# Kernel tuning notes

Measured on AMD Instinct MI355X. Metric: run time of the kernel, lower is better.

The kernel has to match this reference:

```python
import jax, jax.numpy as jnp
import numpy as np

N_HEAD = 16
N_QUERY_GROUPS = 4
HEAD_SIZE = 128
ROPE_N_ELEM = 32
N_EMBD = 2048
LN_EPS = 1e-5


def _layernorm(x, w, b):
    mu = jnp.mean(x, axis=-1, keepdims=True)
    var = jnp.var(x, axis=-1, keepdims=True)
    return (x - mu) * jax.lax.rsqrt(var + LN_EPS) * w + b


def _apply_rope(x, cos, sin):
    # x: (B, H, T, ROPE_N_ELEM); cos/sin: (T, ROPE_N_ELEM) broadcast over B,H
    half = x.shape[-1] // 2
    x1, x2 = x[..., :half], x[..., half:]
    rotated = jnp.concatenate((-x2, x1), axis=-1)
    return x * cos + rotated * sin


def setup_inputs() -> dict:
    key = jax.random.key(0)
    ks = jax.random.split(key, 12)
    B, T, C = 2, 2048, N_EMBD
    qkv_out = (N_HEAD + 2 * N_QUERY_GROUPS) * HEAD_SIZE
    ffn = 4 * C
    s = lambda fan_in: 1.0 / np.sqrt(fan_in)
    # rope cache (lit-gpt build_rope_cache, base 10000)
    theta = 1.0 / (10000.0 ** (jnp.arange(0, ROPE_N_ELEM, 2, dtype=jnp.float32) / ROPE_N_ELEM))
    idx_theta = jnp.outer(jnp.arange(T, dtype=jnp.float32), theta)  # (T, ROPE/2)
    idx_theta = jnp.concatenate((idx_theta, idx_theta), axis=-1)    # (T, ROPE)
    return {
        'x': jax.random.normal(ks[0], (B, T, C), dtype=jnp.float32),
        'cos': jnp.cos(idx_theta),
        'sin': jnp.sin(idx_theta),
        'ln1_w': jnp.ones((C,), jnp.float32),
        'ln1_b': jnp.zeros((C,), jnp.float32),
        'w_qkv': jax.random.normal(ks[1], (C, qkv_out), jnp.float32) * s(C),
        'b_qkv': jnp.zeros((qkv_out,), jnp.float32),
        'w_proj': jax.random.normal(ks[2], (C, C), jnp.float32) * s(C),
        'b_proj': jnp.zeros((C,), jnp.float32),
        'ln2_w': jnp.ones((C,), jnp.float32),
        'ln2_b': jnp.zeros((C,), jnp.float32),
        'w_fc1': jax.random.normal(ks[3], (C, ffn), jnp.float32) * s(C),
        'b_fc1': jnp.zeros((ffn,), jnp.float32),
        'w_fc2': jax.random.normal(ks[4], (ffn, C), jnp.float32) * s(ffn),
        'b_fc2': jnp.zeros((C,), jnp.float32),
    }


def reference(x, cos, sin, ln1_w, ln1_b, w_qkv, b_qkv, w_proj, b_proj,
              ln2_w, ln2_b, w_fc1, b_fc1, w_fc2, b_fc2):
    B, T, C = x.shape
    q_per_kv = N_HEAD // N_QUERY_GROUPS
    D = HEAD_SIZE

    # LayerNormLinear: fused LN + QKV projection
    qkv = _layernorm(x, ln1_w, ln1_b) @ w_qkv + b_qkv           # (B,T,(H+2G)*D)
    qkv = qkv.reshape(B, T, N_QUERY_GROUPS, q_per_kv + 2, D)
    qkv = jnp.transpose(qkv, (0, 2, 3, 1, 4))                    # (B,G,q_per_kv+2,T,D)
    q = qkv[:, :, :q_per_kv]                                     # (B,G,q_per_kv,T,D)
    k = qkv[:, :, q_per_kv:q_per_kv + 1]                         # (B,G,1,T,D)
    v = qkv[:, :, q_per_kv + 1:]
    k = jnp.broadcast_to(k, (B, N_QUERY_GROUPS, q_per_kv, T, D))
    v = jnp.broadcast_to(v, (B, N_QUERY_GROUPS, q_per_kv, T, D))
    q = q.reshape(B, N_HEAD, T, D)
    k = k.reshape(B, N_HEAD, T, D)
    v = v.reshape(B, N_HEAD, T, D)

    # inline RoPE on first ROPE_N_ELEM channels
    q = jnp.concatenate((_apply_rope(q[..., :ROPE_N_ELEM], cos, sin), q[..., ROPE_N_ELEM:]), axis=-1)
    k = jnp.concatenate((_apply_rope(k[..., :ROPE_N_ELEM], cos, sin), k[..., ROPE_N_ELEM:]), axis=-1)

    # causal scaled dot-product attention
    scale = 1.0 / jnp.sqrt(jnp.asarray(D, q.dtype))
    scores = jnp.einsum('bhtd,bhsd->bhts', q, k) * scale          # (B,H,T,T)
    causal = jnp.tril(jnp.ones((T, T), dtype=bool))
    scores = jnp.where(causal, scores, jnp.finfo(scores.dtype).min)
    probs = jax.nn.softmax(scores, axis=-1)
    y = jnp.einsum('bhts,bhsd->bhtd', probs, v)                   # (B,H,T,D)
    y = jnp.transpose(y, (0, 2, 1, 3)).reshape(B, T, C)

    h = y @ w_proj + b_proj

    # parallel residual: x + attn + LayerNormMLP(x)
    mlp_in = _layernorm(x, ln2_w, ln2_b)
    mlp = jax.nn.gelu(mlp_in @ w_fc1 + b_fc1, approximate=False) @ w_fc2 + b_fc2
    return mlp + h + x
```

## Files before the change

### kernel.cpp

```cpp
#include <hip/hip_runtime.h>
#include <cstdint>
#include <cstddef>


typedef unsigned short u16;
typedef __bf16 bf16x8 __attribute__((ext_vector_type(8)));
typedef float  f32x4  __attribute__((ext_vector_type(4)));

#define B_      2
#define T_      2048
#define C_      2048
#define NH_     16
#define NG_     4
#define HD_     128
#define QKVO_   3072
#define FFN_    8192
#define ROWS_   4096

__device__ __forceinline__ u16 f2b(float f) {
  union { float f; uint32_t u; } c; c.f = f;
  uint32_t u = c.u;
  return (u16)((u + 0x7fffu + ((u >> 16) & 1u)) >> 16);
}
__device__ __forceinline__ float b2f(u16 h) {
  union { uint32_t u; float f; } c; c.u = ((uint32_t)h) << 16;
  return c.f;
}
__device__ __forceinline__ void load_lds16(const void* g, void* l) {
  __builtin_amdgcn_global_load_lds(
      (const __attribute__((address_space(1))) uint32_t*)g,
      (__attribute__((address_space(3))) uint32_t*)l, 16, 0, 0);
}

__global__ __launch_bounds__(256) void ln2x_kernel(
    const float* __restrict__ x,
    const float* __restrict__ w1, const float* __restrict__ b1,
    const float* __restrict__ w2, const float* __restrict__ b2,
    u16* __restrict__ o1, u16* __restrict__ o2)
{
  const int row = blockIdx.x;
  const float4* xr = (const float4*)(x + (size_t)row * C_);
  const int t = threadIdx.x;
  float4 v0 = xr[t];
  float4 v1 = xr[t + 256];
  float s  = v0.x + v0.y + v0.z + v0.w + v1.x + v1.y + v1.z + v1.w;
  float ss = v0.x*v0.x + v0.y*v0.y + v0.z*v0.z + v0.w*v0.w
           + v1.x*v1.x + v1.y*v1.y + v1.z*v1.z + v1.w*v1.w;
#pragma unroll
  for (int o = 32; o; o >>= 1) { s += __shfl_down(s, o); ss += __shfl_down(ss, o); }
  __shared__ float red[8];
  const int w = t >> 6;
  if ((t & 63) == 0) { red[w] = s; red[4 + w] = ss; }
  __syncthreads();
  s  = red[0] + red[1] + red[2] + red[3];
  ss = red[4] + red[5] + red[6] + red[7];
  const float mu   = s * (1.0f / C_);
  const float rstd = rsqrtf(ss * (1.0f / C_) - mu * mu + 1e-5f);

  const float4* W1 = (const float4*)w1; const float4* B1 = (const float4*)b1;
  const float4* W2 = (const float4*)w2; const float4* B2 = (const float4*)b2;
#pragma unroll
  for (int c = 0; c < 2; ++c) {
    const int idx = t + c * 256;
    float4 v = (c == 0) ? v0 : v1;
    float n0 = (v.x - mu) * rstd, n1 = (v.y - mu) * rstd;
    float n2 = (v.z - mu) * rstd, n3 = (v.w - mu) * rstd;
    float4 a1 = W1[idx], c1 = B1[idx], a2 = W2[idx], c2 = B2[idx];
    uint64_t p1 = (uint64_t)f2b(n0*a1.x + c1.x)
                | ((uint64_t)f2b(n1*a1.y + c1.y) << 16)
                | ((uint64_t)f2b(n2*a1.z + c1.z) << 32)
                | ((uint64_t)f2b(n3*a1.w + c1.w) << 48);
    uint64_t p2 = (uint64_t)f2b(n0*a2.x + c2.x)
                | ((uint64_t)f2b(n1*a2.y + c2.y) << 16)
                | ((uint64_t)f2b(n2*a2.z + c2.z) << 32)
                | ((uint64_t)f2b(n3*a2.w + c2.w) << 48);
    ((uint64_t*)o1)[(size_t)row * (C_/4) + idx] = p1;
    ((uint64_t*)o2)[(size_t)row * (C_/4) + idx] = p2;
  }
}

__global__ void tcast_kernel(const float* __restrict__ in, u16* __restrict__ out,
                             int R, int Ccols)
{
  __shared__ float tile[32][33];
  const int c0 = blockIdx.x * 32, r0 = blockIdx.y * 32;
  const int tx = threadIdx.x, ty = threadIdx.y;
#pragma unroll
  for (int i = 0; i < 4; ++i)
    tile[ty + i*8][tx] = in[(size_t)(r0 + ty + i*8) * Ccols + c0 + tx];
  __syncthreads();
#pragma unroll
  for (int i = 0; i < 4; ++i)
    out[(size_t)(c0 + ty + i*8) * R + r0 + tx] = f2b(tile[tx][ty + i*8]);
}

template <int EPI>
__global__ __launch_bounds__(256, 2) void gemm_bt(
    const u16* __restrict__ A, const u16* __restrict__ Bt,
    const float* __restrict__ bias, const float* __restrict__ resid,
    u16* __restrict__ outB, float* __restrict__ outF,
    int M, int N, int K)
{
  __shared__ u16 As[128 * 32];
  __shared__ u16 Bs[128 * 32];
  const int tid = threadIdx.x;
  const int w = tid >> 6, lane = tid & 63, quad = lane >> 4, l16 = lane & 15;
  const int wm = w >> 1, wn = w & 1;
  const int m0 = blockIdx.y * 128, n0 = blockIdx.x * 128;

  const f32x4 vzero = {0.f, 0.f, 0.f, 0.f};
  f32x4 acc[4][4];
#pragma unroll
  for (int i = 0; i < 4; ++i)
#pragma unroll
    for (int j = 0; j < 4; ++j) acc[i][j] = vzero;

  const u16* Ap = A  + (size_t)m0 * K;
  const u16* Bp = Bt + (size_t)n0 * K;
  const int rowS = tid >> 2;
  const int slotS = tid & 3;

  for (int k0 = 0; k0 < K; k0 += 32) {
    __syncthreads();
#pragma unroll
    for (int i = 0; i < 2; ++i) {
      int row = rowS + i * 64;
      int chunk = slotS ^ ((row >> 1) & 3);
      load_lds16(Ap + (size_t)row * K + k0 + chunk * 8, (char*)As + i * 4096 + w * 1024);
      load_lds16(Bp + (size_t)row * K + k0 + chunk * 8, (char*)Bs + i * 4096 + w * 1024);
    }
    __syncthreads();

    bf16x8 af[4], bf[4];
#pragma unroll
    for (int mt = 0; mt < 4; ++mt) {
      int row = wm * 64 + mt * 16 + l16;
      int slot = quad ^ ((row >> 1) & 3);
      af[mt] = *(const bf16x8*)(As + row * 32 + slot * 8);
    }
#pragma unroll
    for (int nt = 0; nt < 4; ++nt) {
      int row = wn * 64 + nt * 16 + l16;
      int slot = quad ^ ((row >> 1) & 3);
      bf[nt] = *(const bf16x8*)(Bs + row * 32 + slot * 8);
    }
#pragma unroll
    for (int mt = 0; mt < 4; ++mt)
#pragma unroll
      for (int nt = 0; nt < 4; ++nt)
        acc[mt][nt] = __builtin_amdgcn_mfma_f32_16x16x32_bf16(af[mt], bf[nt], acc[mt][nt], 0, 0, 0);
  }

#pragma unroll
  for (int mt = 0; mt < 4; ++mt)
#pragma unroll
    for (int nt = 0; nt < 4; ++nt)
#pragma unroll
      for (int r = 0; r < 4; ++r) {
        int row = m0 + wm * 64 + mt * 16 + quad * 4 + r;
        int col = n0 + wn * 64 + nt * 16 + l16;
        float v = acc[mt][nt][r] + bias[col];
        if constexpr (EPI == 1)
          v = 0.5f * v * (1.0f + erff(v * 0.70710678118654752f));
        if constexpr (EPI == 2) {
          v += resid[(size_t)row * N + col];
          outF[(size_t)row * N + col] = v;
        } else {
          outB[(size_t)row * N + col] = f2b(v);
        }
      }
}

__global__ __launch_bounds__(256) void rope_kernel(
    const u16* __restrict__ qkv, const float* __restrict__ cosb,
    const float* __restrict__ sinb, u16* __restrict__ qb, u16* __restrict__ kb)
{
  const int bt = blockIdx.x;
  const int b = bt >> 11, t = bt & 2047;
  const u16* base = qkv + (size_t)bt * QKVO_;
  const int d = threadIdx.x & 127;
  const int half = threadIdx.x >> 7;
  for (int it = 0; it < 10; ++it) {
    const int slot = it * 2 + half;
    int col;
    if (slot < 16) {
      int g = slot >> 2, s = slot & 3;
      col = g * 768 + s * 128 + d;
    } else {
      col = (slot - 16) * 768 + 512 + d;
    }
    float v = b2f(base[col]);
    if (d < 32) {
      float cs = cosb[t * 32 + d], sn = sinb[t * 32 + d];
      if (d < 16) v = v * cs - b2f(base[col + 16]) * sn;
      else        v = v * cs + b2f(base[col - 16]) * sn;
    }
    if (slot < 16)
      qb[((size_t)(b * NH_ + slot) * T_ + t) * HD_ + d] = f2b(v);
    else
      kb[((size_t)(b * NG_ + (slot - 16)) * T_ + t) * HD_ + d] = f2b(v);
  }
}

__global__ void vtrans_kernel(const u16* __restrict__ qkv, u16* __restrict__ vtb)
{
  __shared__ u16 tile[32][33];
  const int bg = blockIdx.z, b = bg >> 2, g = bg & 3;
  const int t0 = blockIdx.x * 32, d0 = blockIdx.y * 32;
  const int tx = threadIdx.x, ty = threadIdx.y;
#pragma unroll
  for (int i = 0; i < 4; ++i)
    tile[ty + i*8][tx] =
        qkv[(size_t)(b * T_ + t0 + ty + i*8) * QKVO_ + g * 768 + 640 + d0 + tx];
  __syncthreads();
#pragma unroll
  for (int i = 0; i < 4; ++i)
    vtb[((size_t)(b * NG_ + g) * HD_ + d0 + ty + i*8) * T_ + t0 + tx] =
        tile[tx][ty + i*8];
}

__global__ __launch_bounds__(256, 2) void attn_kernel(
    const u16* __restrict__ qb, const u16* __restrict__ kb,
    const u16* __restrict__ vt, u16* __restrict__ y)
{
  __shared__ u16 Qs[64 * 128];
  __shared__ u16 Ks[64 * 128];
  __shared__ u16 Vs[128 * 64];
  __shared__ u16 Ps[4 * 16 * 64];

  const int tid = threadIdx.x;
  const int w = tid >> 6, lane = tid & 63, quad = lane >> 4, l16 = lane & 15;
  const int b = blockIdx.y >> 4, h = blockIdx.y & 15, g = h >> 2;
  const int q0 = blockIdx.x * 64;

  const u16* Qg = qb + (size_t)(b * NH_ + h) * T_ * HD_;
  const u16* Kg = kb + (size_t)(b * NG_ + g) * T_ * HD_;
  const u16* Vg = vt + (size_t)(b * NG_ + g) * HD_ * T_;

  {
    const int row = tid >> 4, slot = tid & 15;
#pragma unroll
    for (int i = 0; i < 4; ++i) {
      int r = row + i * 16;
      int chunk = slot ^ (r & 7);
      load_lds16(Qg + (size_t)(q0 + r) * HD_ + chunk * 8, (char*)Qs + i * 4096 + w * 1024);
    }
  }

  const f32x4 vzero = {0.f, 0.f, 0.f, 0.f};
  float m_run[4] = {-1e30f, -1e30f, -1e30f, -1e30f};
  float l_run[4] = {0.f, 0.f, 0.f, 0.f};
  f32x4 O[8];
#pragma unroll
  for (int nt = 0; nt < 8; ++nt) O[nt] = vzero;

  const float scale = 0.08838834764831845f;
  const int rowK = tid >> 4, slotK = tid & 15;
  const int rowV = tid >> 3, slotV = tid & 7;

  for (int j = 0; j <= (int)blockIdx.x; ++j) {
    const int kv0 = j * 64;
    __syncthreads();
#pragma unroll
    for (int i = 0; i < 4; ++i) {
      int r = rowK + i * 16;
      int chunk = slotK ^ (r & 7);
      load_lds16(Kg + (size_t)(kv0 + r) * HD_ + chunk * 8, (char*)Ks + i * 4096 + w * 1024);
    }
#pragma unroll
    for (int i = 0; i < 4; ++i) {
      int r = rowV + i * 32;
      int chunk = slotV ^ (r & 7);
      load_lds16(Vg + (size_t)r * T_ + kv0 + chunk * 8, (char*)Vs + i * 4096 + w * 1024);
    }
    __syncthreads();

    bf16x8 aq[4];
#pragma unroll
    for (int kk = 0; kk < 4; ++kk) {
      int row = w * 16 + l16;
      int slot = (kk * 4 + quad) ^ (row & 7);
      aq[kk] = *(const bf16x8*)(Qs + row * 128 + slot * 8);
    }
    f32x4 S[4];
#pragma unroll
    for (int jn = 0; jn < 4; ++jn) {
      f32x4 a = vzero;
#pragma unroll
      for (int kk = 0; kk < 4; ++kk) {
        int row = jn * 16 + l16;
        int slot = (kk * 4 + quad) ^ (row & 7);
        bf16x8 bk = *(const bf16x8*)(Ks + row * 128 + slot * 8);
        a = __builtin_amdgcn_mfma_f32_16x16x32_bf16(aq[kk], bk, a, 0, 0, 0);
      }
      S[jn] = a;
    }

#pragma unroll
    for (int jn = 0; jn < 4; ++jn) {
      int col = kv0 + jn * 16 + l16;
#pragma unroll
      for (int r = 0; r < 4; ++r) {
        int qrow = q0 + w * 16 + quad * 4 + r;
        float v = S[jn][r] * scale;
        S[jn][r] = (col <= qrow) ? v : -1e30f;
      }
    }

    float mx[4];
#pragma unroll
    for (int r = 0; r < 4; ++r)
      mx[r] = fmaxf(fmaxf(S[0][r], S[1][r]), fmaxf(S[2][r], S[3][r]));
#pragma unroll
    for (int d = 1; d < 16; d <<= 1)
#pragma unroll
      for (int r = 0; r < 4; ++r) mx[r] = fmaxf(mx[r], __shfl_xor(mx[r], d));

    float alpha[4];
#pragma unroll
    for (int r = 0; r < 4; ++r) {
      float mn = fmaxf(m_run[r], mx[r]);
      alpha[r] = __expf(m_run[r] - mn);
      m_run[r] = mn;
    }
    float rs[4] = {0.f, 0.f, 0.f, 0.f};
#pragma unroll
    for (int jn = 0; jn < 4; ++jn)
#pragma unroll
      for (int r = 0; r < 4; ++r) {
        float p = __expf(S[jn][r] - m_run[r]);
        S[jn][r] = p;
        rs[r] += p;
      }
#pragma unroll
    for (int d = 1; d < 16; d <<= 1)
#pragma unroll
      for (int r = 0; r < 4; ++r) rs[r] += __shfl_xor(rs[r], d);
#pragma unroll
    for (int r = 0; r < 4; ++r) l_run[r] = l_run[r] * alpha[r] + rs[r];
#pragma unroll
    for (int nt = 0; nt < 8; ++nt)
#pragma unroll
      for (int r = 0; r < 4; ++r) O[nt][r] *= alpha[r];

#pragma unroll
    for (int jn = 0; jn < 4; ++jn)
#pragma unroll
      for (int r = 0; r < 4; ++r) {
        int row = quad * 4 + r;
        int col = jn * 16 + l16;
        int slot = (col >> 3) ^ (row & 7);
        Ps[w * 1024 + row * 64 + slot * 8 + (col & 7)] = f2b(S[jn][r]);
      }

    bf16x8 ap[2];
#pragma unroll
    for (int kk = 0; kk < 2; ++kk) {
      int slot = (kk * 4 + quad) ^ (l16 & 7);
      ap[kk] = *(const bf16x8*)(Ps + w * 1024 + l16 * 64 + slot * 8);
    }
#pragma unroll
    for (int nt = 0; nt < 8; ++nt) {
#pragma unroll
      for (int kk = 0; kk < 2; ++kk) {
        int row = nt * 16 + l16;
        int slot = (kk * 4 + quad) ^ (row & 7);
        bf16x8 bv = *(const bf16x8*)(Vs + row * 64 + slot * 8);
        O[nt] = __builtin_amdgcn_mfma_f32_16x16x32_bf16(ap[kk], bv, O[nt], 0, 0, 0);
      }
    }
  }

#pragma unroll
  for (int r = 0; r < 4; ++r) {
    float inv = 1.0f / l_run[r];
    int t = q0 + w * 16 + quad * 4 + r;
    size_t base = (size_t)(b * T_ + t) * C_ + h * HD_;
#pragma unroll
    for (int nt = 0; nt < 8; ++nt)
      y[base + nt * 16 + l16] = f2b(O[nt][r] * inv);
  }
}

extern "C" void kernel_launch(void* const* d_in, const int* in_sizes, int n_in,
                              void* d_out, int out_size, void* d_ws, size_t ws_size,
                              hipStream_t stream)
{
  const float* x     = (const float*)d_in[0];
  const float* cosb  = (const float*)d_in[1];
  const float* sinb  = (const float*)d_in[2];
  const float* ln1w  = (const float*)d_in[3];
  const float* ln1b  = (const float*)d_in[4];
  const float* wqkv  = (const float*)d_in[5];
  const float* bqkv  = (const float*)d_in[6];
  const float* wproj = (const float*)d_in[7];
  const float* bproj = (const float*)d_in[8];
  const float* ln2w  = (const float*)d_in[9];
  const float* ln2b  = (const float*)d_in[10];
  const float* wfc1  = (const float*)d_in[11];
  const float* bfc1  = (const float*)d_in[12];
  const float* wfc2  = (const float*)d_in[13];
  const float* bfc2  = (const float*)d_in[14];
  float* out = (float*)d_out;

  char* ws = (char*)d_ws;
  size_t off = 0;
  auto alloc = [&](size_t bytes) -> char* {
    char* p = ws + off;
    off += (bytes + 255) & ~(size_t)255;
    return p;
  };
  u16* ln1    = (u16*)alloc((size_t)ROWS_ * C_ * 2);
  u16* ln2    = (u16*)alloc((size_t)ROWS_ * C_ * 2);
  u16* wqkvT  = (u16*)alloc((size_t)QKVO_ * C_ * 2);
  u16* wprojT = (u16*)alloc((size_t)C_ * C_ * 2);
  u16* wfc1T  = (u16*)alloc((size_t)FFN_ * C_ * 2);
  u16* wfc2T  = (u16*)alloc((size_t)C_ * FFN_ * 2);
  u16* qkv    = (u16*)alloc((size_t)ROWS_ * QKVO_ * 2);
  u16* qbuf   = (u16*)alloc((size_t)B_ * NH_ * T_ * HD_ * 2);
  u16* kbuf   = (u16*)alloc((size_t)B_ * NG_ * T_ * HD_ * 2);
  u16* vtb    = (u16*)alloc((size_t)B_ * NG_ * HD_ * T_ * 2);
  u16* ybuf   = (u16*)alloc((size_t)ROWS_ * C_ * 2);
  u16* gbuf   = (u16*)alloc((size_t)ROWS_ * FFN_ * 2);
  if (off > ws_size) return;

  ln2x_kernel<<<dim3(ROWS_), dim3(256), 0, stream>>>(x, ln1w, ln1b, ln2w, ln2b, ln1, ln2);

  dim3 tb(32, 8);
  tcast_kernel<<<dim3(QKVO_/32, C_/32), tb, 0, stream>>>(wqkv, wqkvT, C_, QKVO_);
  tcast_kernel<<<dim3(C_/32,   C_/32), tb, 0, stream>>>(wproj, wprojT, C_, C_);
  tcast_kernel<<<dim3(FFN_/32, C_/32), tb, 0, stream>>>(wfc1, wfc1T, C_, FFN_);
  tcast_kernel<<<dim3(C_/32, FFN_/32), tb, 0, stream>>>(wfc2, wfc2T, FFN_, C_);

  gemm_bt<0><<<dim3(QKVO_/128, ROWS_/128), dim3(256), 0, stream>>>(
      ln1, wqkvT, bqkv, nullptr, qkv, nullptr, ROWS_, QKVO_, C_);

  rope_kernel<<<dim3(ROWS_), dim3(256), 0, stream>>>(qkv, cosb, sinb, qbuf, kbuf);
  vtrans_kernel<<<dim3(T_/32, HD_/32, B_*NG_), tb, 0, stream>>>(qkv, vtb);

  attn_kernel<<<dim3(T_/64, B_*NH_), dim3(256), 0, stream>>>(qbuf, kbuf, vtb, ybuf);

  gemm_bt<2><<<dim3(C_/128, ROWS_/128), dim3(256), 0, stream>>>(
      ybuf, wprojT, bproj, x, nullptr, out, ROWS_, C_, C_);

  gemm_bt<1><<<dim3(FFN_/128, ROWS_/128), dim3(256), 0, stream>>>(
      ln2, wfc1T, bfc1, nullptr, gbuf, nullptr, ROWS_, FFN_, C_);

  gemm_bt<2><<<dim3(C_/128, ROWS_/128), dim3(256), 0, stream>>>(
      gbuf, wfc2T, bfc2, out, nullptr, out, ROWS_, C_, FFN_);
}
```

Before: 944.3 us.

## Fuse RoPE and V-transpose into QKV GEMM epilogue, split-K FC2, faster weight transpose

The QKV GEMM epilogue now applies bias and RoPE and writes Q, K and transposed V directly, which removes the separate rope and vtrans kernels and the intermediate qkv buffer. The FC2 GEMM uses a two-way split-K into a partial buffer (aliased over the ln1/ln2 workspace) followed by an add kernel, to fill more CUs. Weight transpose-cast uses 64x64 tiles with vectorized loads and stores. The attention kernel hoists the Q fragment loads out of the KV loop and applies the causal mask only on the diagonal block. Together these add an extra partial-sum pass over the output and rely on workspace aliasing.

```diff
diff --git a/kernel.cpp b/kernel.cpp
--- a/kernel.cpp
+++ b/kernel.cpp
@@ -79,48 +79,48 @@
   }
 }
 
-__global__ void tcast_kernel(const float* __restrict__ in, u16* __restrict__ out,
-                             int R, int Ccols)
-{
-  __shared__ float tile[32][33];
-  const int c0 = blockIdx.x * 32, r0 = blockIdx.y * 32;
-  const int tx = threadIdx.x, ty = threadIdx.y;
-#pragma unroll
-  for (int i = 0; i < 4; ++i)
-    tile[ty + i*8][tx] = in[(size_t)(r0 + ty + i*8) * Ccols + c0 + tx];
+__global__ __launch_bounds__(256) void tcast64(
+    const float* __restrict__ in, u16* __restrict__ out, int R, int Ccols)
+{
+  __shared__ u16 tileT[64 * 72];
+  const int c0 = blockIdx.x * 64, r0 = blockIdx.y * 64;
+  const int lin = threadIdx.x;
+  {
+    const int cI = (lin & 15) * 4, r = lin >> 4;
+#pragma unroll
+    for (int i = 0; i < 4; ++i) {
+      const int rr = r + i * 16;
+      float4 v = *(const float4*)(in + (size_t)(r0 + rr) * Ccols + c0 + cI);
+      tileT[(cI + 0) * 72 + rr] = f2b(v.x);
+      tileT[(cI + 1) * 72 + rr] = f2b(v.y);
+      tileT[(cI + 2) * 72 + rr] = f2b(v.z);
+      tileT[(cI + 3) * 72 + rr] = f2b(v.w);
+    }
+  }
   __syncthreads();
-#pragma unroll
-  for (int i = 0; i < 4; ++i)
-    out[(size_t)(c0 + ty + i*8) * R + r0 + tx] = f2b(tile[tx][ty + i*8]);
-}
-
-template <int EPI>
-__global__ __launch_bounds__(256, 2) void gemm_bt(
-    const u16* __restrict__ A, const u16* __restrict__ Bt,
-    const float* __restrict__ bias, const float* __restrict__ resid,
-    u16* __restrict__ outB, float* __restrict__ outF,
-    int M, int N, int K)
+  {
+    const int rr = (lin & 15) * 4, cc = lin >> 4;
+#pragma unroll
+    for (int i = 0; i < 4; ++i) {
+      const int c = cc + i * 16;
+      ushort4 pk = *(const ushort4*)(tileT + c * 72 + rr);
+      *(ushort4*)(out + (size_t)(c0 + c) * R + r0 + rr) = pk;
+    }
+  }
+}
+
+__device__ __forceinline__ void gemm_loop(
+    const u16* __restrict__ Ap, const u16* __restrict__ Bp,
+    int K, int kbeg, int kend, f32x4 acc[4][4])
 {
   __shared__ u16 As[128 * 32];
   __shared__ u16 Bs[128 * 32];
   const int tid = threadIdx.x;
   const int w = tid >> 6, lane = tid & 63, quad = lane >> 4, l16 = lane & 15;
   const int wm = w >> 1, wn = w & 1;
-  const int m0 = blockIdx.y * 128, n0 = blockIdx.x * 128;
-
-  const f32x4 vzero = {0.f, 0.f, 0.f, 0.f};
-  f32x4 acc[4][4];
-#pragma unroll
-  for (int i = 0; i < 4; ++i)
-#pragma unroll
-    for (int j = 0; j < 4; ++j) acc[i][j] = vzero;
-
-  const u16* Ap = A  + (size_t)m0 * K;
-  const u16* Bp = Bt + (size_t)n0 * K;
-  const int rowS = tid >> 2;
-  const int slotS = tid & 3;
-
-  for (int k0 = 0; k0 < K; k0 += 32) {
+  const int rowS = tid >> 2, slotS = tid & 3;
+
+  for (int k0 = kbeg; k0 < kend; k0 += 32) {
     __syncthreads();
 #pragma unroll
     for (int i = 0; i < 2; ++i) {
@@ -150,7 +150,104 @@
       for (int nt = 0; nt < 4; ++nt)
         acc[mt][nt] = __builtin_amdgcn_mfma_f32_16x16x32_bf16(af[mt], bf[nt], acc[mt][nt], 0, 0, 0);
   }
-
+}
+
+#define GEMM_PROLOGUE(KSTRIDE, KBEG, KEND)                                    \
+  const int tid = threadIdx.x;                                                \
+  const int w = tid >> 6, lane = tid & 63, quad = lane >> 4, l16 = lane & 15; \
+  const int wm = w >> 1, wn = w & 1;                                          \
+  const int m0 = blockIdx.y * 128, n0 = blockIdx.x * 128;                     \
+  const f32x4 vzero = {0.f, 0.f, 0.f, 0.f};                                   \
+  f32x4 acc[4][4];                                                            \
+  _Pragma("unroll") for (int i = 0; i < 4; ++i)                               \
+    _Pragma("unroll") for (int j = 0; j < 4; ++j) acc[i][j] = vzero;          \
+  gemm_loop(A + (size_t)m0 * (KSTRIDE), Bt + (size_t)n0 * (KSTRIDE),          \
+            (KSTRIDE), (KBEG), (KEND), acc);
+
+__global__ __launch_bounds__(256, 2) void gemm_qkv(
+    const u16* __restrict__ A, const u16* __restrict__ Bt,
+    const float* __restrict__ bias,
+    const float* __restrict__ cosb, const float* __restrict__ sinb,
+    u16* __restrict__ qb, u16* __restrict__ kb, u16* __restrict__ vtb)
+{
+  GEMM_PROLOGUE(C_, 0, C_)
+  const int slice = n0 >> 7;
+  const int g = slice / 6, s = slice % 6;
+  const int b = m0 >> 11;
+
+#pragma unroll
+  for (int mt = 0; mt < 4; ++mt) {
+    const int rowbase = m0 + wm * 64 + mt * 16 + quad * 4;
+    const int t0 = rowbase & 2047;
+    float vv[4][4];
+#pragma unroll
+    for (int nt = 0; nt < 4; ++nt)
+#pragma unroll
+      for (int r = 0; r < 4; ++r)
+        vv[nt][r] = acc[mt][nt][r] + bias[n0 + wn * 64 + nt * 16 + l16];
+
+    if (s < 5 && wn == 0) {
+#pragma unroll
+      for (int r = 0; r < 4; ++r) {
+        const int t = t0 + r;
+        float cs0 = cosb[t * 32 + l16],      sn0 = sinb[t * 32 + l16];
+        float cs1 = cosb[t * 32 + 16 + l16], sn1 = sinb[t * 32 + 16 + l16];
+        float a = vv[0][r], c = vv[1][r];
+        vv[0][r] = a * cs0 - c * sn0;
+        vv[1][r] = c * cs1 + a * sn1;
+      }
+    }
+
+    if (s < 4) {
+      u16* dst = qb + (size_t)(b * NH_ + g * 4 + s) * T_ * HD_;
+#pragma unroll
+      for (int nt = 0; nt < 4; ++nt)
+#pragma unroll
+        for (int r = 0; r < 4; ++r)
+          dst[(size_t)(t0 + r) * HD_ + wn * 64 + nt * 16 + l16] = f2b(vv[nt][r]);
+    } else if (s == 4) {
+      u16* dst = kb + (size_t)(b * NG_ + g) * T_ * HD_;
+#pragma unroll
+      for (int nt = 0; nt < 4; ++nt)
+#pragma unroll
+        for (int r = 0; r < 4; ++r)
+          dst[(size_t)(t0 + r) * HD_ + wn * 64 + nt * 16 + l16] = f2b(vv[nt][r]);
+    } else {
+      u16* dst = vtb + (size_t)(b * NG_ + g) * HD_ * T_;
+#pragma unroll
+      for (int nt = 0; nt < 4; ++nt) {
+        const int d = wn * 64 + nt * 16 + l16;
+        ushort4 pk = { f2b(vv[nt][0]), f2b(vv[nt][1]), f2b(vv[nt][2]), f2b(vv[nt][3]) };
+        *(ushort4*)(dst + (size_t)d * T_ + t0) = pk;
+      }
+    }
+  }
+}
+
+__global__ __launch_bounds__(256, 2) void gemm_proj(
+    const u16* __restrict__ A, const u16* __restrict__ Bt,
+    const float* __restrict__ bias, const float* __restrict__ resid,
+    float* __restrict__ outF)
+{
+  GEMM_PROLOGUE(C_, 0, C_)
+#pragma unroll
+  for (int mt = 0; mt < 4; ++mt)
+#pragma unroll
+    for (int nt = 0; nt < 4; ++nt)
+#pragma unroll
+      for (int r = 0; r < 4; ++r) {
+        int row = m0 + wm * 64 + mt * 16 + quad * 4 + r;
+        int col = n0 + wn * 64 + nt * 16 + l16;
+        float v = acc[mt][nt][r] + bias[col] + resid[(size_t)row * C_ + col];
+        outF[(size_t)row * C_ + col] = v;
+      }
+}
+
+__global__ __launch_bounds__(256, 2) void gemm_fc1(
+    const u16* __restrict__ A, const u16* __restrict__ Bt,
+    const float* __restrict__ bias, u16* __restrict__ outB)
+{
+  GEMM_PROLOGUE(C_, 0, C_)
 #pragma unroll
   for (int mt = 0; mt < 4; ++mt)
 #pragma unroll
@@ -160,63 +257,43 @@
         int row = m0 + wm * 64 + mt * 16 + quad * 4 + r;
         int col = n0 + wn * 64 + nt * 16 + l16;
         float v = acc[mt][nt][r] + bias[col];
-        if constexpr (EPI == 1)
-          v = 0.5f * v * (1.0f + erff(v * 0.70710678118654752f));
-        if constexpr (EPI == 2) {
-          v += resid[(size_t)row * N + col];
-          outF[(size_t)row * N + col] = v;
-        } else {
-          outB[(size_t)row * N + col] = f2b(v);
-        }
-      }
-}
-
-__global__ __launch_bounds__(256) void rope_kernel(
-    const u16* __restrict__ qkv, const float* __restrict__ cosb,
-    const float* __restrict__ sinb, u16* __restrict__ qb, u16* __restrict__ kb)
-{
-  const int bt = blockIdx.x;
-  const int b = bt >> 11, t = bt & 2047;
-  const u16* base = qkv + (size_t)bt * QKVO_;
-  const int d = threadIdx.x & 127;
-  const int half = threadIdx.x >> 7;
-  for (int it = 0; it < 10; ++it) {
-    const int slot = it * 2 + half;
-    int col;
-    if (slot < 16) {
-      int g = slot >> 2, s = slot & 3;
-      col = g * 768 + s * 128 + d;
-    } else {
-      col = (slot - 16) * 768 + 512 + d;
-    }
-    float v = b2f(base[col]);
-    if (d < 32) {
-      float cs = cosb[t * 32 + d], sn = sinb[t * 32 + d];
-      if (d < 16) v = v * cs - b2f(base[col + 16]) * sn;
-      else        v = v * cs + b2f(base[col - 16]) * sn;
-    }
-    if (slot < 16)
-      qb[((size_t)(b * NH_ + slot) * T_ + t) * HD_ + d] = f2b(v);
-    else
-      kb[((size_t)(b * NG_ + (slot - 16)) * T_ + t) * HD_ + d] = f2b(v);
-  }
-}
-
-__global__ void vtrans_kernel(const u16* __restrict__ qkv, u16* __restrict__ vtb)
-{
-  __shared__ u16 tile[32][33];
-  const int bg = blockIdx.z, b = bg >> 2, g = bg & 3;
-  const int t0 = blockIdx.x * 32, d0 = blockIdx.y * 32;
-  const int tx = threadIdx.x, ty = threadIdx.y;
-#pragma unroll
-  for (int i = 0; i < 4; ++i)
-    tile[ty + i*8][tx] =
-        qkv[(size_t)(b * T_ + t0 + ty + i*8) * QKVO_ + g * 768 + 640 + d0 + tx];
-  __syncthreads();
-#pragma unroll
-  for (int i = 0; i < 4; ++i)
-    vtb[((size_t)(b * NG_ + g) * HD_ + d0 + ty + i*8) * T_ + t0 + tx] =
-        tile[tx][ty + i*8];
+        v = 0.5f * v * (1.0f + erff(v * 0.70710678118654752f));
+        outB[(size_t)row * FFN_ + col] = f2b(v);
+      }
+}
+
+__global__ __launch_bounds__(256, 2) void gemm_fc2(
+    const u16* __restrict__ A, const u16* __restrict__ Bt,
+    const float* __restrict__ bias, float* __restrict__ outF,
+    float* __restrict__ pbuf)
+{
+  const int kh = FFN_ / 2;
+  const int kbeg = blockIdx.z * kh;
+  GEMM_PROLOGUE(FFN_, kbeg, kbeg + kh)
+#pragma unroll
+  for (int mt = 0; mt < 4; ++mt)
+#pragma unroll
+    for (int nt = 0; nt < 4; ++nt)
+#pragma unroll
+      for (int r = 0; r < 4; ++r) {
+        int row = m0 + wm * 64 + mt * 16 + quad * 4 + r;
+        int col = n0 + wn * 64 + nt * 16 + l16;
+        size_t idx = (size_t)row * C_ + col;
+        if (blockIdx.z == 0)
+          outF[idx] = acc[mt][nt][r] + bias[col] + outF[idx];
+        else
+          pbuf[idx] = acc[mt][nt][r];
+      }
+}
+
+__global__ __launch_bounds__(256) void add_pbuf(
+    float* __restrict__ out, const float* __restrict__ p)
+{
+  size_t i = ((size_t)blockIdx.x * 256 + threadIdx.x) * 4;
+  float4 a = *(float4*)(out + i);
+  float4 b = *(const float4*)(p + i);
+  a.x += b.x; a.y += b.y; a.z += b.z; a.w += b.w;
+  *(float4*)(out + i) = a;
 }
 
 __global__ __launch_bounds__(256, 2) void attn_kernel(
@@ -246,6 +323,15 @@
       load_lds16(Qg + (size_t)(q0 + r) * HD_ + chunk * 8, (char*)Qs + i * 4096 + w * 1024);
     }
   }
+  __syncthreads();
+
+  bf16x8 aq[4];
+#pragma unroll
+  for (int kk = 0; kk < 4; ++kk) {
+    int row = w * 16 + l16;
+    int slot = (kk * 4 + quad) ^ (row & 7);
+    aq[kk] = *(const bf16x8*)(Qs + row * 128 + slot * 8);
+  }
 
   const f32x4 vzero = {0.f, 0.f, 0.f, 0.f};
   float m_run[4] = {-1e30f, -1e30f, -1e30f, -1e30f};
@@ -275,13 +361,6 @@
     }
     __syncthreads();
 
-    bf16x8 aq[4];
-#pragma unroll
-    for (int kk = 0; kk < 4; ++kk) {
-      int row = w * 16 + l16;
-      int slot = (kk * 4 + quad) ^ (row & 7);
-      aq[kk] = *(const bf16x8*)(Qs + row * 128 + slot * 8);
-    }
     f32x4 S[4];
 #pragma unroll
     for (int jn = 0; jn < 4; ++jn) {
@@ -296,15 +375,22 @@
       S[jn] = a;
     }
 
-#pragma unroll
-    for (int jn = 0; jn < 4; ++jn) {
-      int col = kv0 + jn * 16 + l16;
-#pragma unroll
-      for (int r = 0; r < 4; ++r) {
-        int qrow = q0 + w * 16 + quad * 4 + r;
-        float v = S[jn][r] * scale;
-        S[jn][r] = (col <= qrow) ? v : -1e30f;
-      }
+    if (j == (int)blockIdx.x) {
+#pragma unroll
+      for (int jn = 0; jn < 4; ++jn) {
+        int col = kv0 + jn * 16 + l16;
+#pragma unroll
+        for (int r = 0; r < 4; ++r) {
+          int qrow = q0 + w * 16 + quad * 4 + r;
+          float v = S[jn][r] * scale;
+          S[jn][r] = (col <= qrow) ? v : -1e30f;
+        }
+      }
+    } else {
+#pragma unroll
+      for (int jn = 0; jn < 4; ++jn)
+#pragma unroll
+        for (int r = 0; r < 4; ++r) S[jn][r] *= scale;
     }
 
     float mx[4];
@@ -404,19 +490,20 @@
   float* out = (float*)d_out;
 
   char* ws = (char*)d_ws;
-  size_t off = 0;
+  const size_t MiB = 1ull << 20;
+  u16*   ln1    = (u16*)  (ws + 0);
+  u16*   ln2    = (u16*)  (ws + 16 * MiB);
+  float* pbuf   = (float*)(ws + 0);
+  size_t off = 32 * MiB;
   auto alloc = [&](size_t bytes) -> char* {
     char* p = ws + off;
     off += (bytes + 255) & ~(size_t)255;
     return p;
   };
-  u16* ln1    = (u16*)alloc((size_t)ROWS_ * C_ * 2);
-  u16* ln2    = (u16*)alloc((size_t)ROWS_ * C_ * 2);
   u16* wqkvT  = (u16*)alloc((size_t)QKVO_ * C_ * 2);
   u16* wprojT = (u16*)alloc((size_t)C_ * C_ * 2);
   u16* wfc1T  = (u16*)alloc((size_t)FFN_ * C_ * 2);
   u16* wfc2T  = (u16*)alloc((size_t)C_ * FFN_ * 2);
-  u16* qkv    = (u16*)alloc((size_t)ROWS_ * QKVO_ * 2);
   u16* qbuf   = (u16*)alloc((size_t)B_ * NH_ * T_ * HD_ * 2);
   u16* kbuf   = (u16*)alloc((size_t)B_ * NG_ * T_ * HD_ * 2);
   u16* vtb    = (u16*)alloc((size_t)B_ * NG_ * HD_ * T_ * 2);
@@ -426,26 +513,24 @@
 
   ln2x_kernel<<<dim3(ROWS_), dim3(256), 0, stream>>>(x, ln1w, ln1b, ln2w, ln2b, ln1, ln2);
 
-  dim3 tb(32, 8);
-  tcast_kernel<<<dim3(QKVO_/32, C_/32), tb, 0, stream>>>(wqkv, wqkvT, C_, QKVO_);
-  tcast_kernel<<<dim3(C_/32,   C_/32), tb, 0, stream>>>(wproj, wprojT, C_, C_);
-  tcast_kernel<<<dim3(FFN_/32, C_/32), tb, 0, stream>>>(wfc1, wfc1T, C_, FFN_);
-  tcast_kernel<<<dim3(C_/32, FFN_/32), tb, 0, stream>>>(wfc2, wfc2T, FFN_, C_);
-
-  gemm_bt<0><<<dim3(QKVO_/128, ROWS_/128), dim3(256), 0, stream>>>(
-      ln1, wqkvT, bqkv, nullptr, qkv, nullptr, ROWS_, QKVO_, C_);
-
-  rope_kernel<<<dim3(ROWS_), dim3(256), 0, stream>>>(qkv, cosb, sinb, qbuf, kbuf);
-  vtrans_kernel<<<dim3(T_/32, HD_/32, B_*NG_), tb, 0, stream>>>(qkv, vtb);
+  tcast64<<<dim3(QKVO_/64, C_/64),  dim3(256), 0, stream>>>(wqkv,  wqkvT,  C_,   QKVO_);
+  tcast64<<<dim3(C_/64,   C_/64),   dim3(256), 0, stream>>>(wproj, wprojT, C_,   C_);
+  tcast64<<<dim3(FFN_/64, C_/64),   dim3(256), 0, stream>>>(wfc1,  wfc1T,  C_,   FFN_);
+  tcast64<<<dim3(C_/64,   FFN_/64), dim3(256), 0, stream>>>(wfc2,  wfc2T,  FFN_, C_);
+
+  gemm_qkv<<<dim3(QKVO_/128, ROWS_/128), dim3(256), 0, stream>>>(
+      ln1, wqkvT, bqkv, cosb, sinb, qbuf, kbuf, vtb);
 
   attn_kernel<<<dim3(T_/64, B_*NH_), dim3(256), 0, stream>>>(qbuf, kbuf, vtb, ybuf);
 
-  gemm_bt<2><<<dim3(C_/128, ROWS_/128), dim3(256), 0, stream>>>(
-      ybuf, wprojT, bproj, x, nullptr, out, ROWS_, C_, C_);
-
-  gemm_bt<1><<<dim3(FFN_/128, ROWS_/128), dim3(256), 0, stream>>>(
-      ln2, wfc1T, bfc1, nullptr, gbuf, nullptr, ROWS_, FFN_, C_);
-
-  gemm_bt<2><<<dim3(C_/128, ROWS_/128), dim3(256), 0, stream>>>(
-      gbuf, wfc2T, bfc2, out, nullptr, out, ROWS_, C_, FFN_);
-}
+  gemm_proj<<<dim3(C_/128, ROWS_/128), dim3(256), 0, stream>>>(
+      ybuf, wprojT, bproj, x, out);
+
+  gemm_fc1<<<dim3(FFN_/128, ROWS_/128), dim3(256), 0, stream>>>(
+      ln2, wfc1T, bfc1, gbuf);
+
+  gemm_fc2<<<dim3(C_/128, ROWS_/128, 2), dim3(256), 0, stream>>>(
+      gbuf, wfc2T, bfc2, out, pbuf);
+
+  add_pbuf<<<dim3((ROWS_*C_)/1024), dim3(256), 0, stream>>>(out, pbuf);
+}
```

Result: faster. 900.7 us (-4.6%).
